# Kernel optimization log

Hardware: AMD Instinct MI355X
Metric: run time of the kernel (lower is better)

The kernel has to match this reference:

```python
import jax, jax.numpy as jnp
import numpy as np
import math

D_MODEL = 1024
H = 16
D_H = D_MODEL // H
B, T = 1, 4096


def setup_inputs() -> dict:
    key = jax.random.key(0)
    ks = jax.random.split(key, 9)
    s = 1.0 / math.sqrt(D_MODEL)
    return {
        "x": jax.random.normal(ks[0], (B, T, D_MODEL), dtype=jnp.float32),
        "W_q": jax.random.normal(ks[1], (D_MODEL, D_MODEL), dtype=jnp.float32) * s,
        "b_q": jax.random.normal(ks[2], (D_MODEL,), dtype=jnp.float32) * 0.01,
        "W_k": jax.random.normal(ks[3], (D_MODEL, D_MODEL), dtype=jnp.float32) * s,
        "b_k": jax.random.normal(ks[4], (D_MODEL,), dtype=jnp.float32) * 0.01,
        "W_v": jax.random.normal(ks[5], (D_MODEL, D_MODEL), dtype=jnp.float32) * s,
        "b_v": jax.random.normal(ks[6], (D_MODEL,), dtype=jnp.float32) * 0.01,
        "W_o": jax.random.normal(ks[7], (D_MODEL, D_MODEL), dtype=jnp.float32) * s,
        "b_o": jax.random.normal(ks[8], (D_MODEL,), dtype=jnp.float32) * 0.01,
    }


def reference(x, W_q, b_q, W_k, b_k, W_v, b_v, W_o, b_o):
    b, t, _ = x.shape
    # torch nn.Linear: y = x @ W.T + b
    Q = x @ W_q.T + b_q  # (B, T, d_model)
    K = x @ W_k.T + b_k
    V = x @ W_v.T + b_v
    # split heads -> (B, h, T, d_h)
    Q = Q.reshape(b, t, H, D_H).transpose(0, 2, 1, 3)
    K = K.reshape(b, t, H, D_H).transpose(0, 2, 1, 3)
    V = V.reshape(b, t, H, D_H).transpose(0, 2, 1, 3)
    # scores (B, h, T, T)
    S = jnp.einsum("bhqd,bhkd->bhqk", Q, K) / math.sqrt(D_H)
    # causal mask: disallow k > q
    causal = jnp.tril(jnp.ones((t, t), dtype=bool))  # True = keep
    S = jnp.where(causal, S, -jnp.inf)
    A = jax.nn.softmax(S, axis=-1)
    Y = jnp.einsum("bhqk,bhkd->bhqd", A, V)  # (B, h, T, d_h)
    Y = Y.transpose(0, 2, 1, 3).reshape(b, t, D_MODEL)
    return Y @ W_o.T + b_o
```

## Files before the change

kernel.cpp:

```cpp
#include <hip/hip_runtime.h>


#define TSZ 4096
#define DM  1024
#define NH  16
#define DH  64
#define QSCALE 0.18033688f

typedef __bf16 bf16x8 __attribute__((ext_vector_type(8)));
typedef float  f32x4  __attribute__((ext_vector_type(4)));

__device__ __forceinline__ unsigned short f2bf(float x) {
    __bf16 h = (__bf16)x;
    return __builtin_bit_cast(unsigned short, h);
}

__device__ __forceinline__ uint4 pack8(const float4 a, const float4 b) {
    uint4 r;
    r.x = (unsigned)f2bf(a.x) | ((unsigned)f2bf(a.y) << 16);
    r.y = (unsigned)f2bf(a.z) | ((unsigned)f2bf(a.w) << 16);
    r.z = (unsigned)f2bf(b.x) | ((unsigned)f2bf(b.y) << 16);
    r.w = (unsigned)f2bf(b.z) | ((unsigned)f2bf(b.w) << 16);
    return r;
}

__device__ __forceinline__ int sw(int row, int cb) {
    return row * 64 + ((cb ^ ((row & 7) << 4)) >> 1);
}

__device__ __forceinline__ void gll16(const unsigned short* g, unsigned short* l) {
    __builtin_amdgcn_global_load_lds((const __attribute__((address_space(1))) void*)g,
                                     (__attribute__((address_space(3))) void*)l,
                                     16, 0, 0);
}

template <int CTRL>
__device__ __forceinline__ float dpp_f(float v) {
    return __builtin_bit_cast(float,
        __builtin_amdgcn_update_dpp(0, __builtin_bit_cast(int, v), CTRL, 0xF, 0xF, true));
}
__device__ __forceinline__ float red_sum16(float v) {
    v += dpp_f<0xB1>(v);
    v += dpp_f<0x4E>(v);
    v += dpp_f<0x124>(v);
    v += dpp_f<0x128>(v);
    return v;
}

#define XN  4194304u
#define WN  1048576u
__global__ __launch_bounds__(256)
void cvt_kernel(const float* __restrict__ x,  const float* __restrict__ wq,
                const float* __restrict__ wk, const float* __restrict__ wv,
                const float* __restrict__ wo,
                unsigned short* __restrict__ xb,  unsigned short* __restrict__ wqb,
                unsigned short* __restrict__ wkb, unsigned short* __restrict__ wvb,
                unsigned short* __restrict__ wob) {
    size_t e = ((size_t)blockIdx.x * 256 + threadIdx.x) * 8;
    const float* src; unsigned short* dst; size_t off;
    if (e < XN)               { src = x;  dst = xb;  off = e; }
    else if (e < XN + WN)     { src = wq; dst = wqb; off = e - XN; }
    else if (e < XN + 2 * WN) { src = wk; dst = wkb; off = e - XN - WN; }
    else if (e < XN + 3 * WN) { src = wv; dst = wvb; off = e - XN - 2 * WN; }
    else                      { src = wo; dst = wob; off = e - XN - 3 * WN; }
    float4 a = *reinterpret_cast<const float4*>(src + off);
    float4 b = *reinterpret_cast<const float4*>(src + off + 4);
    *reinterpret_cast<uint4*>(dst + off) = pack8(a, b);
}

__global__ __launch_bounds__(256)
void qkv_kernel(const unsigned short* __restrict__ xb,
                const unsigned short* __restrict__ wqb,
                const unsigned short* __restrict__ wkb,
                const unsigned short* __restrict__ wvb,
                const float* __restrict__ bq, const float* __restrict__ bk,
                const float* __restrict__ bv,
                unsigned short* __restrict__ qw,
                unsigned short* __restrict__ kw,
                unsigned short* __restrict__ vtw) {
    const int L = blockIdx.x;
    const int xcd = L & 7, i = L >> 3;
    const int lbx = i % 3, by = i / 3;
    const int bx = xcd * 3 + lbx;
    const int z = bx >> 3;
    const int col0 = (bx & 7) * 128;
    const int row0 = by * 128;

    const unsigned short* W = (z == 0) ? wqb : (z == 1) ? wkb : wvb;
    const float* bias = (z == 0) ? bq : (z == 1) ? bk : bv;
    unsigned short* outp = (z == 0) ? qw : (z == 1) ? kw : vtw;
    const float scale = (z == 0) ? QSCALE : 1.0f;

    __shared__ unsigned short Al[128 * 64];
    __shared__ unsigned short Bl[128 * 64];

    const int tid = threadIdx.x;
    const int wid = tid >> 6, lane = tid & 63, g = lane >> 4, l15 = lane & 15;
    const int wr = (wid >> 1) * 64, wc = (wid & 1) * 64;

    f32x4 acc[4][4];
#pragma unroll
    for (int m = 0; m < 4; ++m)
#pragma unroll
        for (int n = 0; n < 4; ++n) acc[m][n] = (f32x4){0.f, 0.f, 0.f, 0.f};

    const int r_ = tid >> 3, c8_ = tid & 7;
    const int cbyte = (c8_ * 16) ^ ((r_ & 7) << 4);
    const unsigned short* ga0 = xb + (size_t)(row0 + r_) * DM + (cbyte >> 1);
    const unsigned short* gb0 = W + (size_t)(col0 + r_) * DM + (cbyte >> 1);
    unsigned short* la0 = &Al[(size_t)(wid * 64) * 8];
    unsigned short* lb0 = &Bl[(size_t)(wid * 64) * 8];

    for (int kt = 0; kt < DM; kt += 64) {
#pragma unroll
        for (int is = 0; is < 4; ++is) {
            gll16(ga0 + (size_t)(is * 32) * DM + kt, la0 + (size_t)(is * 256) * 8);
            gll16(gb0 + (size_t)(is * 32) * DM + kt, lb0 + (size_t)(is * 256) * 8);
        }
        __syncthreads();
#pragma unroll
        for (int kk = 0; kk < 2; ++kk) {
            bf16x8 a[4], b[4];
#pragma unroll
            for (int m = 0; m < 4; ++m)
                a[m] = *reinterpret_cast<const bf16x8*>(&Al[sw(wr + m * 16 + l15, kk * 64 + 16 * g)]);
#pragma unroll
            for (int n = 0; n < 4; ++n)
                b[n] = *reinterpret_cast<const bf16x8*>(&Bl[sw(wc + n * 16 + l15, kk * 64 + 16 * g)]);
            if (z == 2) {
#pragma unroll
                for (int m = 0; m < 4; ++m)
#pragma unroll
                    for (int n = 0; n < 4; ++n)
                        acc[m][n] = __builtin_amdgcn_mfma_f32_16x16x32_bf16(b[n], a[m], acc[m][n], 0, 0, 0);
            } else {
#pragma unroll
                for (int m = 0; m < 4; ++m)
#pragma unroll
                    for (int n = 0; n < 4; ++n)
                        acc[m][n] = __builtin_amdgcn_mfma_f32_16x16x32_bf16(a[m], b[n], acc[m][n], 0, 0, 0);
            }
        }
        __syncthreads();
    }

    if (z == 2) {
#pragma unroll
        for (int n = 0; n < 4; ++n)
#pragma unroll
            for (int r = 0; r < 4; ++r) {
                int ch = col0 + wc + n * 16 + 4 * g + r;
                float bval = bias[ch];
#pragma unroll
                for (int m = 0; m < 4; ++m) {
                    int t = row0 + wr + m * 16 + l15;
                    outp[(size_t)ch * TSZ + t] = f2bf(acc[m][n][r] + bval);
                }
            }
    } else {
#pragma unroll
        for (int n = 0; n < 4; ++n) {
            int col = col0 + wc + n * 16 + l15;
            float bval = bias[col];
            int hh = col >> 6, dd = col & 63;
#pragma unroll
            for (int m = 0; m < 4; ++m) {
                int rbase = row0 + wr + m * 16 + 4 * g;
#pragma unroll
                for (int r = 0; r < 4; ++r)
                    outp[((size_t)hh * TSZ + rbase + r) * DH + dd] = f2bf((acc[m][n][r] + bval) * scale);
            }
        }
    }
}

__global__ __launch_bounds__(256)
void attn_kernel(const unsigned short* __restrict__ qw,
                 const unsigned short* __restrict__ kw,
                 const unsigned short* __restrict__ vtw,
                 unsigned short* __restrict__ yw) {
    __shared__ unsigned short Qs[64 * 64];
    __shared__ unsigned short Ks[2][64 * 64];
    __shared__ unsigned short Vs[2][64 * 64];
    __shared__ unsigned short Ps[64 * 64];

    const int L = blockIdx.x;
    const int xcd = L & 7, k = L >> 3;
    const int h = xcd + 8 * (k & 1);
    const int qt = 63 - (k >> 1);
    const int tid = threadIdx.x;
    const int wid = tid >> 6, lane = tid & 63, g = lane >> 4, l15 = lane & 15;

    const unsigned short* qbase = qw + (size_t)h * TSZ * DH;
    const unsigned short* kbase = kw + (size_t)h * TSZ * DH;
    const unsigned short* vbase = vtw + (size_t)h * DH * TSZ;

    {
        const unsigned short* qsrc = qbase + (size_t)qt * 64 * DH;
#pragma unroll
        for (int i2 = 0; i2 < 2; ++i2) {
            int c = tid + i2 * 256;
            int r = c >> 3, c8 = c & 7;
            *reinterpret_cast<uint4*>(&Qs[sw(r, c8 * 16)]) =
                *reinterpret_cast<const uint4*>(qsrc + c * 8);
            *reinterpret_cast<uint4*>(&Ks[0][sw(r, c8 * 16)]) =
                *reinterpret_cast<const uint4*>(kbase + c * 8);
            *reinterpret_cast<uint4*>(&Vs[0][sw(r, c8 * 16)]) =
                *reinterpret_cast<const uint4*>(vbase + (size_t)r * TSZ + c8 * 8);
        }
    }
    __syncthreads();

    bf16x8 aq[2];
    aq[0] = *reinterpret_cast<const bf16x8*>(&Qs[sw(wid * 16 + l15, 16 * g)]);
    aq[1] = *reinterpret_cast<const bf16x8*>(&Qs[sw(wid * 16 + l15, 64 + 16 * g)]);

    float l_st[4];
    f32x4 accO[4];
#pragma unroll
    for (int r = 0; r < 4; ++r) l_st[r] = 0.f;
#pragma unroll
    for (int n = 0; n < 4; ++n) accO[n] = (f32x4){0.f, 0.f, 0.f, 0.f};

    for (int j = 0; j <= qt; ++j) {
        const int cur = j & 1;
        const bool pf = (j < qt);
        uint4 pk0, pk1, pv0, pv1;
        if (pf) {
            const unsigned short* ks = kbase + (size_t)(j + 1) * 64 * DH;
            const unsigned short* vs = vbase + (size_t)(j + 1) * 64;
            int c0 = tid, c1 = tid + 256;
            pk0 = *reinterpret_cast<const uint4*>(ks + c0 * 8);
            pk1 = *reinterpret_cast<const uint4*>(ks + c1 * 8);
            pv0 = *reinterpret_cast<const uint4*>(vs + (size_t)(c0 >> 3) * TSZ + (c0 & 7) * 8);
            pv1 = *reinterpret_cast<const uint4*>(vs + (size_t)(c1 >> 3) * TSZ + (c1 & 7) * 8);
        }

        f32x4 sacc[4];
#pragma unroll
        for (int n = 0; n < 4; ++n) sacc[n] = (f32x4){0.f, 0.f, 0.f, 0.f};
        __builtin_amdgcn_s_setprio(1);
#pragma unroll
        for (int kk = 0; kk < 2; ++kk) {
#pragma unroll
            for (int n = 0; n < 4; ++n) {
                bf16x8 bk = *reinterpret_cast<const bf16x8*>(&Ks[cur][sw(n * 16 + l15, kk * 64 + 16 * g)]);
                sacc[n] = __builtin_amdgcn_mfma_f32_16x16x32_bf16(aq[kk], bk, sacc[n], 0, 0, 0);
            }
        }
        __builtin_amdgcn_s_setprio(0);
        if (j == qt) {
#pragma unroll
            for (int n = 0; n < 4; ++n)
#pragma unroll
                for (int r = 0; r < 4; ++r)
                    if (n * 16 + l15 > wid * 16 + 4 * g + r) sacc[n][r] = -__builtin_inff();
        }

        float p[4][4];
#pragma unroll
        for (int r = 0; r < 4; ++r) {
            float rs = 0.f;
#pragma unroll
            for (int n = 0; n < 4; ++n) { p[n][r] = exp2f(sacc[n][r]); rs += p[n][r]; }
            l_st[r] += rs;
        }

#pragma unroll
        for (int n = 0; n < 4; ++n)
#pragma unroll
            for (int r = 0; r < 4; ++r)
                Ps[sw(wid * 16 + 4 * g + r, (n * 16 + l15) * 2)] = f2bf(p[n][r]);

        if (pf) {
            int c0 = tid, c1 = tid + 256;
            *reinterpret_cast<uint4*>(&Ks[cur ^ 1][sw(c0 >> 3, (c0 & 7) * 16)]) = pk0;
            *reinterpret_cast<uint4*>(&Ks[cur ^ 1][sw(c1 >> 3, (c1 & 7) * 16)]) = pk1;
            *reinterpret_cast<uint4*>(&Vs[cur ^ 1][sw(c0 >> 3, (c0 & 7) * 16)]) = pv0;
            *reinterpret_cast<uint4*>(&Vs[cur ^ 1][sw(c1 >> 3, (c1 & 7) * 16)]) = pv1;
        }

        __builtin_amdgcn_s_setprio(1);
#pragma unroll
        for (int kk = 0; kk < 2; ++kk) {
            bf16x8 pa = *reinterpret_cast<const bf16x8*>(&Ps[sw(wid * 16 + l15, kk * 64 + 16 * g)]);
#pragma unroll
            for (int n = 0; n < 4; ++n) {
                bf16x8 bv = *reinterpret_cast<const bf16x8*>(&Vs[cur][sw(n * 16 + l15, kk * 64 + 16 * g)]);
                accO[n] = __builtin_amdgcn_mfma_f32_16x16x32_bf16(pa, bv, accO[n], 0, 0, 0);
            }
        }
        __builtin_amdgcn_s_setprio(0);
        __syncthreads();
    }

#pragma unroll
    for (int r = 0; r < 4; ++r) {
        float lt = red_sum16(l_st[r]);
        float inv = 1.0f / lt;
        int row = qt * 64 + wid * 16 + 4 * g + r;
#pragma unroll
        for (int n = 0; n < 4; ++n)
            yw[(size_t)row * DM + h * DH + n * 16 + l15] = f2bf(accO[n][r] * inv);
    }
}

__global__ __launch_bounds__(256)
void oproj_kernel(const unsigned short* __restrict__ y,
                  const unsigned short* __restrict__ wob,
                  const float* __restrict__ bo,
                  float* __restrict__ out) {
    const int L = blockIdx.x;
    const int xcd = L & 7, i = L >> 3;
    const int bx = i & 7, lby = i >> 3;
    const int by = xcd * 4 + lby;
    const int row0 = by * 128, col0 = bx * 128;

    __shared__ unsigned short Al[128 * 64];
    __shared__ unsigned short Bl[128 * 64];

    const int tid = threadIdx.x;
    const int wid = tid >> 6, lane = tid & 63, g = lane >> 4, l15 = lane & 15;
    const int wr = (wid >> 1) * 64, wc = (wid & 1) * 64;

    f32x4 acc[4][4];
#pragma unroll
    for (int m = 0; m < 4; ++m)
#pragma unroll
        for (int n = 0; n < 4; ++n) acc[m][n] = (f32x4){0.f, 0.f, 0.f, 0.f};

    const int r_ = tid >> 3, c8_ = tid & 7;
    const int cbyte = (c8_ * 16) ^ ((r_ & 7) << 4);
    const unsigned short* ga0 = y + (size_t)(row0 + r_) * DM + (cbyte >> 1);
    const unsigned short* gb0 = wob + (size_t)(col0 + r_) * DM + (cbyte >> 1);
    unsigned short* la0 = &Al[(size_t)(wid * 64) * 8];
    unsigned short* lb0 = &Bl[(size_t)(wid * 64) * 8];

    for (int kt = 0; kt < DM; kt += 64) {
#pragma unroll
        for (int is = 0; is < 4; ++is) {
            gll16(ga0 + (size_t)(is * 32) * DM + kt, la0 + (size_t)(is * 256) * 8);
            gll16(gb0 + (size_t)(is * 32) * DM + kt, lb0 + (size_t)(is * 256) * 8);
        }
        __syncthreads();
#pragma unroll
        for (int kk = 0; kk < 2; ++kk) {
            bf16x8 a[4], b[4];
#pragma unroll
            for (int m = 0; m < 4; ++m)
                a[m] = *reinterpret_cast<const bf16x8*>(&Al[sw(wr + m * 16 + l15, kk * 64 + 16 * g)]);
#pragma unroll
            for (int n = 0; n < 4; ++n)
                b[n] = *reinterpret_cast<const bf16x8*>(&Bl[sw(wc + n * 16 + l15, kk * 64 + 16 * g)]);
#pragma unroll
            for (int m = 0; m < 4; ++m)
#pragma unroll
                for (int n = 0; n < 4; ++n)
                    acc[m][n] = __builtin_amdgcn_mfma_f32_16x16x32_bf16(a[m], b[n], acc[m][n], 0, 0, 0);
        }
        __syncthreads();
    }

#pragma unroll
    for (int n = 0; n < 4; ++n) {
        int col = col0 + wc + n * 16 + l15;
        float bval = bo[col];
#pragma unroll
        for (int m = 0; m < 4; ++m) {
            int rbase = row0 + wr + m * 16 + 4 * g;
#pragma unroll
            for (int r = 0; r < 4; ++r)
                out[(size_t)(rbase + r) * DM + col] = acc[m][n][r] + bval;
        }
    }
}

extern "C" void kernel_launch(void* const* d_in, const int* in_sizes, int n_in,
                              void* d_out, int out_size, void* d_ws, size_t ws_size,
                              hipStream_t stream) {
    const float* x  = (const float*)d_in[0];
    const float* Wq = (const float*)d_in[1];
    const float* bq = (const float*)d_in[2];
    const float* Wk = (const float*)d_in[3];
    const float* bk = (const float*)d_in[4];
    const float* Wv = (const float*)d_in[5];
    const float* bv = (const float*)d_in[6];
    const float* Wo = (const float*)d_in[7];
    const float* bo = (const float*)d_in[8];
    float* out = (float*)d_out;

    unsigned short* xb  = (unsigned short*)d_ws;
    unsigned short* wqb = xb + 4194304;
    unsigned short* wkb = wqb + 1048576;
    unsigned short* wvb = wkb + 1048576;
    unsigned short* wob = wvb + 1048576;
    unsigned short* qw  = wob + 1048576;
    unsigned short* kw  = qw + 4194304;
    unsigned short* vtw = kw + 4194304;
    unsigned short* yw  = xb;

    cvt_kernel<<<4096, 256, 0, stream>>>(x, Wq, Wk, Wv, Wo, xb, wqb, wkb, wvb, wob);
    qkv_kernel<<<768, 256, 0, stream>>>(xb, wqb, wkb, wvb, bq, bk, bv, qw, kw, vtw);
    attn_kernel<<<1024, 256, 0, stream>>>(qw, kw, vtw, yw);
    oproj_kernel<<<256, 256, 0, stream>>>(yw, wob, bo, out);
}
```

Measured before the change: 143.9 us.

## Process 128-key tiles per attention iteration with single-buffered K/V

The causal attention loop now handles 128 keys per iteration instead of 64, which halves the number of iterations and their per-iteration overhead. K and V drop from double-buffered LDS to single-buffered, with register prefetch followed by two barriers per iteration, and Q is staged through the P buffer. The mask for the final tile is computed in absolute positions, so an odd tile count gives a half-masked final tile. The exchange is an extra barrier per iteration, higher register use (8 score accumulators, 8 prefetch registers) and some wasted work on the masked half tile.

```diff
diff --git a/kernel.cpp b/kernel.cpp
--- a/kernel.cpp
+++ b/kernel.cpp
@@ -26,6 +26,9 @@
 
 __device__ __forceinline__ int sw(int row, int cb) {
     return row * 64 + ((cb ^ ((row & 7) << 4)) >> 1);
+}
+__device__ __forceinline__ int sw128(int row, int cb) {
+    return row * 128 + ((cb ^ ((row & 7) << 4)) >> 1);
 }
 
 __device__ __forceinline__ void gll16(const unsigned short* g, unsigned short* l) {
@@ -179,10 +182,9 @@
                  const unsigned short* __restrict__ kw,
                  const unsigned short* __restrict__ vtw,
                  unsigned short* __restrict__ yw) {
-    __shared__ unsigned short Qs[64 * 64];
-    __shared__ unsigned short Ks[2][64 * 64];
-    __shared__ unsigned short Vs[2][64 * 64];
-    __shared__ unsigned short Ps[64 * 64];
+    __shared__ unsigned short Ks[128 * 64];
+    __shared__ unsigned short Vs[64 * 128];
+    __shared__ unsigned short Ps[64 * 128];
 
     const int L = blockIdx.x;
     const int xcd = L & 7, k = L >> 3;
@@ -195,25 +197,40 @@
     const unsigned short* kbase = kw + (size_t)h * TSZ * DH;
     const unsigned short* vbase = vtw + (size_t)h * DH * TSZ;
 
+    const int NT = (qt + 2) >> 1;
+
+    int okl[4], ovl[4], vr[4], vc[4];
+#pragma unroll
+    for (int i2 = 0; i2 < 4; ++i2) {
+        int c = tid + i2 * 256;
+        okl[i2] = sw(c >> 3, (c & 7) * 16);
+        vr[i2] = c >> 4; vc[i2] = (c & 15) * 8;
+        ovl[i2] = sw128(vr[i2], vc[i2] * 2);
+    }
+
     {
         const unsigned short* qsrc = qbase + (size_t)qt * 64 * DH;
 #pragma unroll
         for (int i2 = 0; i2 < 2; ++i2) {
             int c = tid + i2 * 256;
-            int r = c >> 3, c8 = c & 7;
-            *reinterpret_cast<uint4*>(&Qs[sw(r, c8 * 16)]) =
+            *reinterpret_cast<uint4*>(&Ps[sw(c >> 3, (c & 7) * 16)]) =
                 *reinterpret_cast<const uint4*>(qsrc + c * 8);
-            *reinterpret_cast<uint4*>(&Ks[0][sw(r, c8 * 16)]) =
+        }
+#pragma unroll
+        for (int i2 = 0; i2 < 4; ++i2) {
+            int c = tid + i2 * 256;
+            *reinterpret_cast<uint4*>(&Ks[okl[i2]]) =
                 *reinterpret_cast<const uint4*>(kbase + c * 8);
-            *reinterpret_cast<uint4*>(&Vs[0][sw(r, c8 * 16)]) =
-                *reinterpret_cast<const uint4*>(vbase + (size_t)r * TSZ + c8 * 8);
+            *reinterpret_cast<uint4*>(&Vs[ovl[i2]]) =
+                *reinterpret_cast<const uint4*>(vbase + (size_t)vr[i2] * TSZ + vc[i2]);
         }
     }
     __syncthreads();
 
     bf16x8 aq[2];
-    aq[0] = *reinterpret_cast<const bf16x8*>(&Qs[sw(wid * 16 + l15, 16 * g)]);
-    aq[1] = *reinterpret_cast<const bf16x8*>(&Qs[sw(wid * 16 + l15, 64 + 16 * g)]);
+    aq[0] = *reinterpret_cast<const bf16x8*>(&Ps[sw(wid * 16 + l15, 16 * g)]);
+    aq[1] = *reinterpret_cast<const bf16x8*>(&Ps[sw(wid * 16 + l15, 64 + 16 * g)]);
+    __syncthreads();
 
     float l_st[4];
     f32x4 accO[4];
@@ -222,76 +239,76 @@
 #pragma unroll
     for (int n = 0; n < 4; ++n) accO[n] = (f32x4){0.f, 0.f, 0.f, 0.f};
 
-    for (int j = 0; j <= qt; ++j) {
-        const int cur = j & 1;
-        const bool pf = (j < qt);
-        uint4 pk0, pk1, pv0, pv1;
+    for (int jj = 0; jj < NT; ++jj) {
+        const bool pf = (jj + 1 < NT);
+        uint4 pk[4], pv[4];
         if (pf) {
-            const unsigned short* ks = kbase + (size_t)(j + 1) * 64 * DH;
-            const unsigned short* vs = vbase + (size_t)(j + 1) * 64;
-            int c0 = tid, c1 = tid + 256;
-            pk0 = *reinterpret_cast<const uint4*>(ks + c0 * 8);
-            pk1 = *reinterpret_cast<const uint4*>(ks + c1 * 8);
-            pv0 = *reinterpret_cast<const uint4*>(vs + (size_t)(c0 >> 3) * TSZ + (c0 & 7) * 8);
-            pv1 = *reinterpret_cast<const uint4*>(vs + (size_t)(c1 >> 3) * TSZ + (c1 & 7) * 8);
-        }
-
-        f32x4 sacc[4];
-#pragma unroll
-        for (int n = 0; n < 4; ++n) sacc[n] = (f32x4){0.f, 0.f, 0.f, 0.f};
+            const unsigned short* ks = kbase + (size_t)(jj + 1) * 128 * DH;
+            const unsigned short* vs = vbase + (size_t)(jj + 1) * 128;
+#pragma unroll
+            for (int i2 = 0; i2 < 4; ++i2) {
+                int c = tid + i2 * 256;
+                pk[i2] = *reinterpret_cast<const uint4*>(ks + c * 8);
+                pv[i2] = *reinterpret_cast<const uint4*>(vs + (size_t)vr[i2] * TSZ + vc[i2]);
+            }
+        }
+
+        f32x4 sacc[8];
+#pragma unroll
+        for (int n = 0; n < 8; ++n) sacc[n] = (f32x4){0.f, 0.f, 0.f, 0.f};
         __builtin_amdgcn_s_setprio(1);
 #pragma unroll
         for (int kk = 0; kk < 2; ++kk) {
 #pragma unroll
-            for (int n = 0; n < 4; ++n) {
-                bf16x8 bk = *reinterpret_cast<const bf16x8*>(&Ks[cur][sw(n * 16 + l15, kk * 64 + 16 * g)]);
+            for (int n = 0; n < 8; ++n) {
+                bf16x8 bk = *reinterpret_cast<const bf16x8*>(&Ks[sw(n * 16 + l15, kk * 64 + 16 * g)]);
                 sacc[n] = __builtin_amdgcn_mfma_f32_16x16x32_bf16(aq[kk], bk, sacc[n], 0, 0, 0);
             }
         }
         __builtin_amdgcn_s_setprio(0);
-        if (j == qt) {
-#pragma unroll
-            for (int n = 0; n < 4; ++n)
+        if (jj == NT - 1) {
+#pragma unroll
+            for (int n = 0; n < 8; ++n)
 #pragma unroll
                 for (int r = 0; r < 4; ++r)
-                    if (n * 16 + l15 > wid * 16 + 4 * g + r) sacc[n][r] = -__builtin_inff();
-        }
-
-        float p[4][4];
+                    if (jj * 128 + n * 16 + l15 > qt * 64 + wid * 16 + 4 * g + r)
+                        sacc[n][r] = -__builtin_inff();
+        }
+
 #pragma unroll
         for (int r = 0; r < 4; ++r) {
             float rs = 0.f;
-#pragma unroll
-            for (int n = 0; n < 4; ++n) { p[n][r] = exp2f(sacc[n][r]); rs += p[n][r]; }
+            int prow = wid * 16 + 4 * g + r;
+#pragma unroll
+            for (int n = 0; n < 8; ++n) {
+                float pp = exp2f(sacc[n][r]);
+                rs += pp;
+                Ps[sw128(prow, (n * 16 + l15) * 2)] = f2bf(pp);
+            }
             l_st[r] += rs;
         }
 
-#pragma unroll
-        for (int n = 0; n < 4; ++n)
-#pragma unroll
-            for (int r = 0; r < 4; ++r)
-                Ps[sw(wid * 16 + 4 * g + r, (n * 16 + l15) * 2)] = f2bf(p[n][r]);
+        __builtin_amdgcn_s_setprio(1);
+#pragma unroll
+        for (int kk = 0; kk < 4; ++kk) {
+            bf16x8 pa = *reinterpret_cast<const bf16x8*>(&Ps[sw128(wid * 16 + l15, kk * 64 + 16 * g)]);
+#pragma unroll
+            for (int n = 0; n < 4; ++n) {
+                bf16x8 bv = *reinterpret_cast<const bf16x8*>(&Vs[sw128(n * 16 + l15, kk * 64 + 16 * g)]);
+                accO[n] = __builtin_amdgcn_mfma_f32_16x16x32_bf16(pa, bv, accO[n], 0, 0, 0);
+            }
+        }
+        __builtin_amdgcn_s_setprio(0);
 
         if (pf) {
-            int c0 = tid, c1 = tid + 256;
-            *reinterpret_cast<uint4*>(&Ks[cur ^ 1][sw(c0 >> 3, (c0 & 7) * 16)]) = pk0;
-            *reinterpret_cast<uint4*>(&Ks[cur ^ 1][sw(c1 >> 3, (c1 & 7) * 16)]) = pk1;
-            *reinterpret_cast<uint4*>(&Vs[cur ^ 1][sw(c0 >> 3, (c0 & 7) * 16)]) = pv0;
-            *reinterpret_cast<uint4*>(&Vs[cur ^ 1][sw(c1 >> 3, (c1 & 7) * 16)]) = pv1;
-        }
-
-        __builtin_amdgcn_s_setprio(1);
-#pragma unroll
-        for (int kk = 0; kk < 2; ++kk) {
-            bf16x8 pa = *reinterpret_cast<const bf16x8*>(&Ps[sw(wid * 16 + l15, kk * 64 + 16 * g)]);
-#pragma unroll
-            for (int n = 0; n < 4; ++n) {
-                bf16x8 bv = *reinterpret_cast<const bf16x8*>(&Vs[cur][sw(n * 16 + l15, kk * 64 + 16 * g)]);
-                accO[n] = __builtin_amdgcn_mfma_f32_16x16x32_bf16(pa, bv, accO[n], 0, 0, 0);
-            }
-        }
-        __builtin_amdgcn_s_setprio(0);
-        __syncthreads();
+            __syncthreads();
+#pragma unroll
+            for (int i2 = 0; i2 < 4; ++i2) {
+                *reinterpret_cast<uint4*>(&Ks[okl[i2]]) = pk[i2];
+                *reinterpret_cast<uint4*>(&Vs[ovl[i2]]) = pv[i2];
+            }
+            __syncthreads();
+        }
     }
 
 #pragma unroll
```

After: 246.0 us. +70.9%, slower.
